# Performance work log

Hardware: AMD Instinct MI355X
Metric: run time of the kernel (lower is better)

## Reference

```python
import jax, jax.numpy as jnp
import numpy as np

EPS_CR = 0.5      # eps in coding rate
ETA = 0.5
LAMBDA_LAP = 0.3
LN_EPS = 1e-5


def setup_inputs() -> dict:
    key = jax.random.key(0)
    ks = jax.random.split(key, 8)
    n, in_dim, out_dim, d_sub, K1 = 8192, 256, 128, 64, 3
    H = jax.random.normal(ks[0], (n, in_dim), jnp.float32)
    hop_feats = jax.random.normal(ks[1], (K1, n, in_dim), jnp.float32)
    L = jax.random.normal(ks[2], (n, n), jnp.float32) * 0.01
    W_stack = jax.random.normal(ks[3], (K1, d_sub, in_dim), jnp.float32) * 0.05
    W_out = jax.random.normal(ks[4], (out_dim, in_dim), jnp.float32) * 0.05
    threshold = jnp.full((out_dim,), 0.05, jnp.float32)
    ln_gamma = jnp.ones((out_dim,), jnp.float32)
    ln_beta = jnp.zeros((out_dim,), jnp.float32)
    tau = jnp.asarray(1.0, jnp.float32)
    return {"H": H, "hop_feats": hop_feats, "L": L, "W_stack": W_stack,
            "W_out": W_out, "threshold": threshold, "ln_gamma": ln_gamma,
            "ln_beta": ln_beta, "tau": tau}


def reference(H, hop_feats, L, W_stack, W_out, threshold, ln_gamma, ln_beta, tau):
    n = H.shape[0]
    d = W_stack.shape[1]
    coeff = d / (n * EPS_CR * EPS_CR)
    # per-hop subspace projections: Z [K+1, n, d]
    Z = jnp.einsum('knf,kdf->knd', hop_feats, W_stack)
    # shared Gram M = I + coeff * Z^T Z  [K+1, d, d]
    G = jnp.einsum('knd,kne->kde', Z, Z)
    M = jnp.eye(d, dtype=Z.dtype)[None] + coeff * G
    # coding rates via batched slogdet
    _, logdet = jnp.linalg.slogdet(M)
    R = 0.5 * logdet                                    # [K+1]
    # delta_R: first entry is R[0], rest are successive diffs
    delta_R = R - jnp.concatenate([jnp.zeros((1,), R.dtype), R[:-1]])
    dR_norm = (delta_R - delta_R.mean()) / (jnp.std(delta_R, ddof=1) + 1e-6)
    w = jax.nn.softmax(dR_norm / tau)                   # [K+1]
    # coding-rate gradients: g_Z = coeff * Z @ M^{-1} via batched solve
    g_Z = coeff * jnp.linalg.solve(M, jnp.swapaxes(Z, 1, 2))  # [K+1, d, n]
    # g_H[k] = g_Z[k]^T @ W[k]; weighted sum over hops -> [n, in_dim]
    grad_contrib = jnp.einsum('k,kdn,kdf->nf', w, g_Z, W_stack)
    H_half = H + ETA * grad_contrib - ETA * LAMBDA_LAP * (L @ H)
    # in_dim != out_dim -> project
    H_pre = H_half @ W_out.T                            # [n, out_dim]
    thr = jnp.abs(threshold)[None, :]
    H_soft = jnp.sign(H_pre) * jnp.maximum(jnp.abs(H_pre) - thr, 0.0)
    # LayerNorm over last dim
    mu = H_soft.mean(-1, keepdims=True)
    var = jnp.mean((H_soft - mu) ** 2, -1, keepdims=True)
    H_out = (H_soft - mu) * jax.lax.rsqrt(var + LN_EPS) * ln_gamma + ln_beta
    return (H_out, w, jax.lax.stop_gradient(dR_norm), jax.lax.stop_gradient(delta_R))
```

## Files before the change

kernel.cpp:

```cpp
#include <hip/hip_runtime.h>
#include <hip/hip_bf16.h>
#include <math.h>


#define COEFF 0.03125f
#define SCL_LAP (-0.15f)

typedef __attribute__((ext_vector_type(8))) short short8;
typedef __attribute__((ext_vector_type(4))) float f32x4;

__device__ __forceinline__ unsigned short f2bf_bits(float f) {
  unsigned int u = __float_as_uint(f);
  unsigned int r = (u + 0x7fffu + ((u >> 16) & 1u)) >> 16;
  return (unsigned short)r;
}

__device__ __forceinline__ void gemm_body(
    const float* __restrict__ A, const float* __restrict__ B,
    int K, int lda, int ldb, int m0, int n0,
    float* As, float* Bs, float cc[4][4]) {
  const int tid = threadIdx.x;
  const int tx = tid & 15, ty = tid >> 4;
#pragma unroll
  for (int i = 0; i < 4; ++i)
#pragma unroll
    for (int j = 0; j < 4; ++j) cc[i][j] = 0.f;
  const int lr = tid >> 2, lc = (tid & 3) << 2;
  for (int k0 = 0; k0 < K; k0 += 16) {
    float4 av = *(const float4*)(A + (size_t)(m0 + lr) * lda + k0 + lc);
    As[(lc) * 68 + lr] = av.x; As[(lc + 1) * 68 + lr] = av.y;
    As[(lc + 2) * 68 + lr] = av.z; As[(lc + 3) * 68 + lr] = av.w;
    float4 bv = *(const float4*)(B + (size_t)(n0 + lr) * ldb + k0 + lc);
    Bs[(lc) * 68 + lr] = bv.x; Bs[(lc + 1) * 68 + lr] = bv.y;
    Bs[(lc + 2) * 68 + lr] = bv.z; Bs[(lc + 3) * 68 + lr] = bv.w;
    __syncthreads();
#pragma unroll
    for (int kk = 0; kk < 16; ++kk) {
      float4 a4 = *(const float4*)&As[kk * 68 + ty * 4];
      float4 b4 = *(const float4*)&Bs[kk * 68 + tx * 4];
      float a[4] = {a4.x, a4.y, a4.z, a4.w};
      float bb[4] = {b4.x, b4.y, b4.z, b4.w};
#pragma unroll
      for (int i = 0; i < 4; ++i)
#pragma unroll
        for (int j = 0; j < 4; ++j) cc[i][j] = fmaf(a[i], bb[j], cc[i][j]);
    }
    __syncthreads();
  }
}

__global__ __launch_bounds__(256) void front_kernel(
    const float* __restrict__ H, const float* __restrict__ hop,
    const float* __restrict__ Wst, const float* __restrict__ Wout,
    float* __restrict__ Hp, unsigned short* __restrict__ HpT,
    float* __restrict__ Zbuf, float* __restrict__ Gpart,
    float* __restrict__ Pb) {
  __shared__ __align__(16) float smem[4420];
  float* As = smem;
  float* Bs = smem + 1088;
  const int tid = threadIdx.x;
  const int tx = tid & 15, ty = tid >> 4;
  float cc[4][4];
  const int b = blockIdx.x;

  if (b < 256) {
    const int m0 = (b >> 1) * 64, n0 = (b & 1) * 64;
    gemm_body(H, Wout, 256, 256, 256, m0, n0, As, Bs, cc);
#pragma unroll
    for (int i = 0; i < 4; ++i) {
      float4 v = {cc[i][0], cc[i][1], cc[i][2], cc[i][3]};
      *(float4*)(Hp + (size_t)(m0 + ty * 4 + i) * 128 + n0 + tx * 4) = v;
    }
#pragma unroll
    for (int i = 0; i < 4; ++i)
#pragma unroll
      for (int j = 0; j < 4; ++j)
        smem[(ty * 4 + i) * 65 + tx * 4 + j] = cc[i][j];
    __syncthreads();
    const int c = tid >> 2, mb = (tid & 3) << 4;
    __attribute__((aligned(16))) unsigned short tmp[16];
#pragma unroll
    for (int t = 0; t < 16; ++t) tmp[t] = f2bf_bits(smem[(mb + t) * 65 + c]);
    unsigned short* dst = HpT + (size_t)(n0 + c) * 8192 + m0 + mb;
    *(uint4*)dst = *(const uint4*)&tmp[0];
    *(uint4*)(dst + 8) = *(const uint4*)&tmp[8];
  } else if (b < 640) {
    const int i2 = b - 256;
    const int k = i2 >> 7, mblk = i2 & 127;
    const int m0 = mblk * 64;
    gemm_body(hop + (size_t)k * 2097152, Wst + (size_t)k * 16384,
              256, 256, 256, m0, 0, As, Bs, cc);
#pragma unroll
    for (int i = 0; i < 4; ++i) {
      float4 v = {cc[i][0], cc[i][1], cc[i][2], cc[i][3]};
      *(float4*)(Zbuf + (size_t)(m0 + ty * 4 + i) * 192 + k * 64 + tx * 4) = v;
    }
#pragma unroll
    for (int i = 0; i < 4; ++i)
#pragma unroll
      for (int j = 0; j < 4; ++j)
        smem[(ty * 4 + i) * 68 + tx * 4 + j] = cc[i][j];
    __syncthreads();
    float g[4][4];
#pragma unroll
    for (int i = 0; i < 4; ++i)
#pragma unroll
      for (int j = 0; j < 4; ++j) g[i][j] = 0.f;
    const int d0 = tx * 4, e0 = ty * 4;
    for (int r = 0; r < 64; ++r) {
      float4 zd4 = *(const float4*)&smem[r * 68 + d0];
      float4 ze4 = *(const float4*)&smem[r * 68 + e0];
      float zd[4] = {zd4.x, zd4.y, zd4.z, zd4.w};
      float ze[4] = {ze4.x, ze4.y, ze4.z, ze4.w};
#pragma unroll
      for (int i = 0; i < 4; ++i)
#pragma unroll
        for (int j = 0; j < 4; ++j) g[i][j] = fmaf(zd[i], ze[j], g[i][j]);
    }
    float* gp = Gpart + ((size_t)k * 128 + mblk) * 4096;
#pragma unroll
    for (int i = 0; i < 4; ++i) {
      float4 v = {g[i][0], g[i][1], g[i][2], g[i][3]};
      *(float4*)(gp + (d0 + i) * 64 + e0) = v;
    }
  } else {
    const int i2 = b - 640;
    const int k = i2 >> 1;
    const int m0 = (i2 & 1) * 64;
    gemm_body(Wout, Wst + (size_t)k * 16384, 256, 256, 256, m0, 0, As, Bs, cc);
    float* P = Pb + (size_t)k * 8192;
#pragma unroll
    for (int i = 0; i < 4; ++i) {
      float4 v = {cc[i][0], cc[i][1], cc[i][2], cc[i][3]};
      *(float4*)(P + (size_t)(m0 + ty * 4 + i) * 64 + tx * 4) = v;
    }
  }
}

__global__ __launch_bounds__(256) void gsum_kernel(
    const float* __restrict__ Gpart, float* __restrict__ Gsum) {
  const int k = blockIdx.x >> 4;
  const int i = ((blockIdx.x & 15) << 8) + threadIdx.x;
  const float* gp = Gpart + (size_t)k * 128 * 4096 + i;
  float s0 = 0.f, s1 = 0.f, s2 = 0.f, s3 = 0.f;
  for (int bb = 0; bb < 128; bb += 4) {
    s0 += gp[(size_t)bb * 4096];
    s1 += gp[(size_t)(bb + 1) * 4096];
    s2 += gp[(size_t)(bb + 2) * 4096];
    s3 += gp[(size_t)(bb + 3) * 4096];
  }
  Gsum[(size_t)k * 4096 + i] = (s0 + s1) + (s2 + s3);
}

__device__ __forceinline__ float blocksum256(float v, volatile float* scr) {
#pragma unroll
  for (int o = 32; o; o >>= 1) v += __shfl_xor(v, o);
  __syncthreads();
  if ((threadIdx.x & 63) == 0) scr[threadIdx.x >> 6] = v;
  __syncthreads();
  return scr[0] + scr[1] + scr[2] + scr[3];
}

__device__ __forceinline__ void gemm64s(const float* X, const float* Y,
                                        float acc[4][4]) {
  const int tx = threadIdx.x & 15, ty = threadIdx.x >> 4;
#pragma unroll
  for (int i = 0; i < 4; ++i)
#pragma unroll
    for (int j = 0; j < 4; ++j) acc[i][j] = 0.f;
  for (int kk = 0; kk < 64; ++kk) {
    float4 a4 = *(const float4*)&X[kk * 64 + ty * 4];
    float4 b4 = *(const float4*)&Y[kk * 64 + tx * 4];
    float a[4] = {a4.x, a4.y, a4.z, a4.w};
    float bb[4] = {b4.x, b4.y, b4.z, b4.w};
#pragma unroll
    for (int i = 0; i < 4; ++i)
#pragma unroll
      for (int j = 0; j < 4; ++j) acc[i][j] = fmaf(a[i], bb[j], acc[i][j]);
  }
}

__device__ __forceinline__ void wb64(float* D, const float acc[4][4]) {
  const int tx = threadIdx.x & 15, ty = threadIdx.x >> 4;
#pragma unroll
  for (int i = 0; i < 4; ++i)
#pragma unroll
    for (int j = 0; j < 4; ++j) D[(ty * 4 + i) * 64 + tx * 4 + j] = acc[i][j];
}

__device__ __forceinline__ float dot64(const float* X, const float* Y, float* scr) {
  const int tx = threadIdx.x & 15, ty = threadIdx.x >> 4;
  float v = 0.f;
#pragma unroll
  for (int i = 0; i < 4; ++i)
#pragma unroll
    for (int j = 0; j < 4; ++j) {
      int idx = (ty * 4 + i) * 64 + tx * 4 + j;
      v += X[idx] * Y[idx];
    }
  return blocksum256(v, scr);
}

__global__ __launch_bounds__(256) void fused_big(
    const float* __restrict__ Lp, const unsigned short* __restrict__ HpT,
    float* __restrict__ Pbuf, const float* __restrict__ Gsum,
    float* __restrict__ Minv, float* __restrict__ Rout) {
  __shared__ __align__(16) float smem[12304];
  const int tid = threadIdx.x;

  if (blockIdx.x >= 3) {
    unsigned short (*As)[40] = (unsigned short(*)[40])smem;
    unsigned short (*Bs)[40] = (unsigned short(*)[40])(smem + 2560);
    const int g = blockIdx.x - 3;
    const int m0 = (g & 63) * 128;
    const int split = g >> 6;
    const int kbase = split * 1024;
    const int wave = tid >> 6, lane = tid & 63;
    const int ar = tid >> 1, ah = (tid & 1) * 16;
    const size_t lrow = (size_t)(m0 + ar) * 8192;
    const size_t brow = (size_t)ar * 8192;
    f32x4 acc[2][8];
#pragma unroll
    for (int i = 0; i < 2; ++i)
#pragma unroll
      for (int j = 0; j < 8; ++j) acc[i][j] = (f32x4){0.f, 0.f, 0.f, 0.f};
    float4 apf[4];
    uint4 bpf[2];
    {
      const float* ap = Lp + lrow + kbase + ah;
      apf[0] = *(const float4*)(ap); apf[1] = *(const float4*)(ap + 4);
      apf[2] = *(const float4*)(ap + 8); apf[3] = *(const float4*)(ap + 12);
      const unsigned short* bp = HpT + brow + kbase + ah;
      bpf[0] = *(const uint4*)(bp); bpf[1] = *(const uint4*)(bp + 8);
    }
    const int quad = lane >> 4, mcol = lane & 15;
    for (int step = 0; step < 32; ++step) {
      __syncthreads();
      {
        __attribute__((aligned(16))) unsigned short tmp[16];
        const float* f = (const float*)apf;
#pragma unroll
        for (int i = 0; i < 16; ++i) tmp[i] = f2bf_bits(f[i]);
        *(uint4*)&As[ar][ah] = *(const uint4*)&tmp[0];
        *(uint4*)&As[ar][ah + 8] = *(const uint4*)&tmp[8];
        *(uint4*)&Bs[ar][ah] = bpf[0];
        *(uint4*)&Bs[ar][ah + 8] = bpf[1];
      }
      __syncthreads();
      if (step < 31) {
        int kc = kbase + (step + 1) * 32;
        const float* ap = Lp + lrow + kc + ah;
        apf[0] = *(const float4*)(ap); apf[1] = *(const float4*)(ap + 4);
        apf[2] = *(const float4*)(ap + 8); apf[3] = *(const float4*)(ap + 12);
        const unsigned short* bp = HpT + brow + kc + ah;
        bpf[0] = *(const uint4*)(bp); bpf[1] = *(const uint4*)(bp + 8);
      }
      short8 af0 = *(const short8*)&As[wave * 32 + mcol][quad * 8];
      short8 af1 = *(const short8*)&As[wave * 32 + 16 + mcol][quad * 8];
#pragma unroll
      for (int nt = 0; nt < 8; ++nt) {
        short8 bf = *(const short8*)&Bs[nt * 16 + mcol][quad * 8];
        acc[0][nt] = __builtin_amdgcn_mfma_f32_16x16x32_bf16(af0, bf, acc[0][nt], 0, 0, 0);
        acc[1][nt] = __builtin_amdgcn_mfma_f32_16x16x32_bf16(af1, bf, acc[1][nt], 0, 0, 0);
      }
    }
    float* P = Pbuf + (size_t)split * 1048576;
#pragma unroll
    for (int mt = 0; mt < 2; ++mt)
#pragma unroll
      for (int nt = 0; nt < 8; ++nt)
#pragma unroll
        for (int r = 0; r < 4; ++r) {
          int grow = m0 + wave * 32 + mt * 16 + quad * 4 + r;
          int gcol = nt * 16 + mcol;
          P[(size_t)grow * 128 + gcol] = acc[mt][nt][r];
        }
    return;
  }

  const int k = blockIdx.x;
  float* B0 = smem;
  float* B1 = smem + 4096;
  float* B2 = smem + 8192;
  float* scr = smem + 12288;
  for (int i = tid; i < 4096; i += 256) {
    B0[i] = COEFF * Gsum[(size_t)k * 4096 + i] + ((i >> 6) == (i & 63) ? 1.f : 0.f);
  }
  __syncthreads();
  if (tid < 64) {
    float rs = 0.f, dg = B0[tid * 65];
    for (int j = 0; j < 64; ++j) rs += fabsf(B0[j * 64 + tid]);
    float lo = 2.f * dg - rs, hi = rs;
#pragma unroll
    for (int o = 32; o; o >>= 1) {
      lo = fminf(lo, __shfl_xor(lo, o));
      hi = fmaxf(hi, __shfl_xor(hi, o));
    }
    if (tid == 0) scr[4] = 0.5f * (fmaxf(lo, 1.f) + hi);
  }
  __syncthreads();
  const float alpha = scr[4], inva = 1.f / alpha;
  for (int i = tid; i < 4096; i += 256) {
    int r = i >> 6, c = i & 63;
    B0[i] = B0[i] * inva - (r == c ? 1.f : 0.f);
  }
  __syncthreads();
  const int tx = tid & 15, ty = tid >> 4;
  float v1 = 0.f, v2 = 0.f;
#pragma unroll
  for (int i = 0; i < 4; ++i)
#pragma unroll
    for (int j = 0; j < 4; ++j) {
      int r = ty * 4 + i, c = tx * 4 + j;
      float e = B0[r * 64 + c];
      if (r == c) v1 += e;
      v2 += e * e;
    }
  float t1 = blocksum256(v1, scr);
  float t2 = blocksum256(v2, scr);
  float acc[4][4];
  gemm64s(B0, B0, acc); __syncthreads(); wb64(B1, acc); __syncthreads();
  float t3 = dot64(B1, B0, scr);
  float t4 = dot64(B1, B1, scr);
  gemm64s(B1, B0, acc); __syncthreads(); wb64(B2, acc); __syncthreads();
  float t5 = dot64(B2, B1, scr);
  float t6 = dot64(B2, B2, scr);
  gemm64s(B1, B1, acc);
  {
    float v7 = 0.f, v8 = 0.f;
#pragma unroll
    for (int i = 0; i < 4; ++i)
#pragma unroll
      for (int j = 0; j < 4; ++j) {
        int idx = (ty * 4 + i) * 64 + tx * 4 + j;
        v7 += acc[i][j] * B2[idx];
        v8 += acc[i][j] * acc[i][j];
      }
    float t7 = blocksum256(v7, scr);
    float t8 = blocksum256(v8, scr);
    if (tid == 0) {
      float ld = 64.f * logf(alpha) + t1 - t2 * 0.5f + t3 / 3.f - t4 * 0.25f
                 + t5 * 0.2f - t6 / 6.f + t7 / 7.f - t8 * 0.125f;
      Rout[k] = 0.5f * ld;
    }
  }
  for (int i = tid; i < 4096; i += 256) {
    int r = i >> 6, c = i & 63;
    B1[i] = (r == c ? 1.f : 0.f) - B0[i];
  }
  __syncthreads();
  for (int it = 0; it < 2; ++it) {
    gemm64s(B0, B1, acc);
    __syncthreads();
    {
#pragma unroll
      for (int i = 0; i < 4; ++i)
#pragma unroll
        for (int j = 0; j < 4; ++j) {
          int idx = (ty * 4 + i) * 64 + tx * 4 + j;
          B2[idx] = acc[i][j] + B1[idx];
        }
    }
    __syncthreads();
    gemm64s(B1, B2, acc);
    __syncthreads();
    {
#pragma unroll
      for (int i = 0; i < 4; ++i)
#pragma unroll
        for (int j = 0; j < 4; ++j) {
          int idx = (ty * 4 + i) * 64 + tx * 4 + j;
          B1[idx] = 2.f * B1[idx] - acc[i][j];
        }
    }
    __syncthreads();
  }
  for (int i = tid; i < 4096; i += 256) Minv[k * 4096 + i] = B1[i] * inva;
}

__global__ __launch_bounds__(256) void qtw_kernel(
    const float* __restrict__ Pb, const float* __restrict__ Minv,
    const float* __restrict__ R, const float* __restrict__ tauP,
    float* __restrict__ QT, float* __restrict__ tail) {
  __shared__ __align__(16) float XT[4096];
  __shared__ __align__(16) float Y[4096];
  __shared__ float wsh;
  const int tid = threadIdx.x;
  const int k = blockIdx.x >> 1;
  const int m0 = (blockIdx.x & 1) * 64;
  if (tid == 0) {
    float R0 = R[0], R1 = R[1], R2 = R[2];
    float d0 = R0, d1 = R1 - R0, d2 = R2 - R1;
    float mean = (d0 + d1 + d2) * (1.f / 3.f);
    float e0 = d0 - mean, e1 = d1 - mean, e2 = d2 - mean;
    float sd = sqrtf((e0 * e0 + e1 * e1 + e2 * e2) * 0.5f) + 1e-6f;
    float n0 = e0 / sd, n1 = e1 / sd, n2 = e2 / sd;
    float tau = tauP[0];
    float x0 = n0 / tau, x1 = n1 / tau, x2 = n2 / tau;
    float mx = fmaxf(x0, fmaxf(x1, x2));
    float w0 = expf(x0 - mx), w1 = expf(x1 - mx), w2 = expf(x2 - mx);
    float s = w0 + w1 + w2;
    w0 /= s; w1 /= s; w2 /= s;
    wsh = 0.015625f * (k == 0 ? w0 : (k == 1 ? w1 : w2));
    if (blockIdx.x == 0) {
      tail[0] = w0; tail[1] = w1; tail[2] = w2;
      tail[3] = n0; tail[4] = n1; tail[5] = n2;
      tail[6] = d0; tail[7] = d1; tail[8] = d2;
    }
  }
  {
    const int m = tid >> 2, c4 = (tid & 3) << 4;
    const float* src = Pb + (size_t)k * 8192 + (size_t)(m0 + m) * 64 + c4;
#pragma unroll
    for (int t = 0; t < 16; t += 4) {
      float4 v = *(const float4*)(src + t);
      XT[(c4 + t) * 64 + m] = v.x;
      XT[(c4 + t + 1) * 64 + m] = v.y;
      XT[(c4 + t + 2) * 64 + m] = v.z;
      XT[(c4 + t + 3) * 64 + m] = v.w;
    }
    for (int t = tid * 4; t < 4096; t += 1024)
      *(float4*)&Y[t] = *(const float4*)(Minv + (size_t)k * 4096 + t);
  }
  __syncthreads();
  float acc[4][4];
  gemm64s(XT, Y, acc);
  const float s = wsh;
  const int tx = tid & 15, ty = tid >> 4;
#pragma unroll
  for (int i = 0; i < 4; ++i) {
    float4 v = {s * acc[i][0], s * acc[i][1], s * acc[i][2], s * acc[i][3]};
    *(float4*)(QT + (size_t)(m0 + ty * 4 + i) * 192 + k * 64 + tx * 4) = v;
  }
}

__global__ __launch_bounds__(256) void back_kernel(
    const float* __restrict__ Zbuf, const float* __restrict__ QT,
    const float* __restrict__ Hp, const float* __restrict__ Pbuf,
    const float* __restrict__ thr, const float* __restrict__ gamma,
    const float* __restrict__ beta, float* __restrict__ out) {
  __shared__ __align__(16) float As[16][36];
  __shared__ __align__(16) float Bs[16][132];
  const int tid = threadIdx.x;
  const int tx = tid & 15, ty = tid >> 4;
  const int m0 = blockIdx.x * 32;
  float cc[2][8];
#pragma unroll
  for (int i = 0; i < 2; ++i)
#pragma unroll
    for (int j = 0; j < 8; ++j) cc[i][j] = 0.f;
  const int lr = tid >> 2, lc = (tid & 3) << 2;
  const int jr = tid >> 1, jc = (tid & 1) << 3;
  for (int k0 = 0; k0 < 192; k0 += 16) {
    if (tid < 128) {
      float4 av = *(const float4*)(Zbuf + (size_t)(m0 + lr) * 192 + k0 + lc);
      As[lc][lr] = av.x; As[lc + 1][lr] = av.y;
      As[lc + 2][lr] = av.z; As[lc + 3][lr] = av.w;
    }
    {
      const float* q = QT + (size_t)jr * 192 + k0 + jc;
      float4 b0 = *(const float4*)(q);
      float4 b1 = *(const float4*)(q + 4);
      Bs[jc][jr] = b0.x; Bs[jc + 1][jr] = b0.y;
      Bs[jc + 2][jr] = b0.z; Bs[jc + 3][jr] = b0.w;
      Bs[jc + 4][jr] = b1.x; Bs[jc + 5][jr] = b1.y;
      Bs[jc + 6][jr] = b1.z; Bs[jc + 7][jr] = b1.w;
    }
    __syncthreads();
#pragma unroll
    for (int kk = 0; kk < 16; ++kk) {
      float2 a2 = *(const float2*)&As[kk][ty * 2];
      float4 b4a = *(const float4*)&Bs[kk][tx * 8];
      float4 b4b = *(const float4*)&Bs[kk][tx * 8 + 4];
      float bb[8] = {b4a.x, b4a.y, b4a.z, b4a.w, b4b.x, b4b.y, b4b.z, b4b.w};
#pragma unroll
      for (int j = 0; j < 8; ++j) {
        cc[0][j] = fmaf(a2.x, bb[j], cc[0][j]);
        cc[1][j] = fmaf(a2.y, bb[j], cc[1][j]);
      }
    }
    __syncthreads();
  }
  const float4 tA = *(const float4*)(thr + tx * 8);
  const float4 tB = *(const float4*)(thr + tx * 8 + 4);
  const float tv[8] = {fabsf(tA.x), fabsf(tA.y), fabsf(tA.z), fabsf(tA.w),
                       fabsf(tB.x), fabsf(tB.y), fabsf(tB.z), fabsf(tB.w)};
  const float4 gA = *(const float4*)(gamma + tx * 8);
  const float4 gB = *(const float4*)(gamma + tx * 8 + 4);
  const float gv[8] = {gA.x, gA.y, gA.z, gA.w, gB.x, gB.y, gB.z, gB.w};
  const float4 bA = *(const float4*)(beta + tx * 8);
  const float4 bB = *(const float4*)(beta + tx * 8 + 4);
  const float bv[8] = {bA.x, bA.y, bA.z, bA.w, bB.x, bB.y, bB.z, bB.w};
  float sres[2][8], mean[2], inv[2];
#pragma unroll
  for (int i = 0; i < 2; ++i) {
    const size_t off = (size_t)(m0 + ty * 2 + i) * 128 + tx * 8;
    float4 h0 = *(const float4*)(Hp + off);
    float4 h1 = *(const float4*)(Hp + off + 4);
    float p[8] = {0.f, 0.f, 0.f, 0.f, 0.f, 0.f, 0.f, 0.f};
#pragma unroll
    for (int sp = 0; sp < 8; ++sp) {
      const float* pb = Pbuf + (size_t)sp * 1048576 + off;
      float4 q0 = *(const float4*)(pb);
      float4 q1 = *(const float4*)(pb + 4);
      p[0] += q0.x; p[1] += q0.y; p[2] += q0.z; p[3] += q0.w;
      p[4] += q1.x; p[5] += q1.y; p[6] += q1.z; p[7] += q1.w;
    }
    const float hv[8] = {h0.x, h0.y, h0.z, h0.w, h1.x, h1.y, h1.z, h1.w};
    float sum = 0.f;
#pragma unroll
    for (int j = 0; j < 8; ++j) {
      float x = cc[i][j] + hv[j] + SCL_LAP * p[j];
      float a = fmaxf(fabsf(x) - tv[j], 0.f);
      float sx = (x >= 0.f) ? a : -a;
      sres[i][j] = sx;
      sum += sx;
    }
#pragma unroll
    for (int o = 1; o < 16; o <<= 1) sum += __shfl_xor(sum, o);
    mean[i] = sum * (1.f / 128.f);
    float ss = 0.f;
#pragma unroll
    for (int j = 0; j < 8; ++j) {
      float dd = sres[i][j] - mean[i];
      ss += dd * dd;
    }
#pragma unroll
    for (int o = 1; o < 16; o <<= 1) ss += __shfl_xor(ss, o);
    inv[i] = rsqrtf(ss * (1.f / 128.f) + 1e-5f);
  }
#pragma unroll
  for (int i = 0; i < 2; ++i) {
    const size_t off = (size_t)(m0 + ty * 2 + i) * 128 + tx * 8;
    float o8[8];
#pragma unroll
    for (int j = 0; j < 8; ++j)
      o8[j] = (sres[i][j] - mean[i]) * inv[i] * gv[j] + bv[j];
    float4 v0 = {o8[0], o8[1], o8[2], o8[3]};
    float4 v1 = {o8[4], o8[5], o8[6], o8[7]};
    *(float4*)(out + off) = v0;
    *(float4*)(out + off + 4) = v1;
  }
}

extern "C" void kernel_launch(void* const* d_in, const int* in_sizes, int n_in,
                              void* d_out, int out_size, void* d_ws, size_t ws_size,
                              hipStream_t stream) {
  const float* H = (const float*)d_in[0];
  const float* hop = (const float*)d_in[1];
  const float* L = (const float*)d_in[2];
  const float* Wst = (const float*)d_in[3];
  const float* Wout = (const float*)d_in[4];
  const float* thr = (const float*)d_in[5];
  const float* gamma = (const float*)d_in[6];
  const float* beta = (const float*)d_in[7];
  const float* tau = (const float*)d_in[8];
  float* out = (float*)d_out;

  float* ws = (float*)d_ws;
  float* Zbuf = ws;
  float* Hp = Zbuf + 1572864;
  float* Gpart = Hp + 1048576;
  float* Gsum = Gpart + 1572864;
  float* Minv = Gsum + 12288;
  float* Rb = Minv + 12288;
  float* Pb = Rb + 16;
  float* QT = Pb + 24576;
  float* Pbuf = QT + 24576;
  unsigned short* HpT = (unsigned short*)(Pbuf + 8388608);

  front_kernel<<<dim3(646), 256, 0, stream>>>(H, hop, Wst, Wout,
                                              Hp, HpT, Zbuf, Gpart, Pb);
  gsum_kernel<<<dim3(48), 256, 0, stream>>>(Gpart, Gsum);
  fused_big<<<dim3(515), 256, 0, stream>>>(L, HpT, Pbuf, Gsum, Minv, Rb);
  qtw_kernel<<<dim3(6), 256, 0, stream>>>(Pb, Minv, Rb, tau, QT, out + 1048576);
  back_kernel<<<dim3(256), 256, 0, stream>>>(Zbuf, QT, Hp, Pbuf,
                                             thr, gamma, beta, out);

  (void)in_sizes; (void)n_in; (void)out_size; (void)ws_size;
}
```

Baseline: 493.1 us.

## Enlarge front GEMM tiles, fold Gram partial sum into solver, reorder split-K mapping

```diff
diff --git a/kernel.cpp b/kernel.cpp
--- a/kernel.cpp
+++ b/kernel.cpp
@@ -13,40 +13,6 @@
   unsigned int u = __float_as_uint(f);
   unsigned int r = (u + 0x7fffu + ((u >> 16) & 1u)) >> 16;
   return (unsigned short)r;
-}
-
-__device__ __forceinline__ void gemm_body(
-    const float* __restrict__ A, const float* __restrict__ B,
-    int K, int lda, int ldb, int m0, int n0,
-    float* As, float* Bs, float cc[4][4]) {
-  const int tid = threadIdx.x;
-  const int tx = tid & 15, ty = tid >> 4;
-#pragma unroll
-  for (int i = 0; i < 4; ++i)
-#pragma unroll
-    for (int j = 0; j < 4; ++j) cc[i][j] = 0.f;
-  const int lr = tid >> 2, lc = (tid & 3) << 2;
-  for (int k0 = 0; k0 < K; k0 += 16) {
-    float4 av = *(const float4*)(A + (size_t)(m0 + lr) * lda + k0 + lc);
-    As[(lc) * 68 + lr] = av.x; As[(lc + 1) * 68 + lr] = av.y;
-    As[(lc + 2) * 68 + lr] = av.z; As[(lc + 3) * 68 + lr] = av.w;
-    float4 bv = *(const float4*)(B + (size_t)(n0 + lr) * ldb + k0 + lc);
-    Bs[(lc) * 68 + lr] = bv.x; Bs[(lc + 1) * 68 + lr] = bv.y;
-    Bs[(lc + 2) * 68 + lr] = bv.z; Bs[(lc + 3) * 68 + lr] = bv.w;
-    __syncthreads();
-#pragma unroll
-    for (int kk = 0; kk < 16; ++kk) {
-      float4 a4 = *(const float4*)&As[kk * 68 + ty * 4];
-      float4 b4 = *(const float4*)&Bs[kk * 68 + tx * 4];
-      float a[4] = {a4.x, a4.y, a4.z, a4.w};
-      float bb[4] = {b4.x, b4.y, b4.z, b4.w};
-#pragma unroll
-      for (int i = 0; i < 4; ++i)
-#pragma unroll
-        for (int j = 0; j < 4; ++j) cc[i][j] = fmaf(a[i], bb[j], cc[i][j]);
-    }
-    __syncthreads();
-  }
 }
 
 __global__ __launch_bounds__(256) void front_kernel(
@@ -55,61 +21,80 @@
     float* __restrict__ Hp, unsigned short* __restrict__ HpT,
     float* __restrict__ Zbuf, float* __restrict__ Gpart,
     float* __restrict__ Pb) {
-  __shared__ __align__(16) float smem[4420];
+  __shared__ __align__(16) float smem[8704];
   float* As = smem;
-  float* Bs = smem + 1088;
+  float* Bs = smem + 2112;
   const int tid = threadIdx.x;
   const int tx = tid & 15, ty = tid >> 4;
-  float cc[4][4];
   const int b = blockIdx.x;
 
-  if (b < 256) {
-    const int m0 = (b >> 1) * 64, n0 = (b & 1) * 64;
-    gemm_body(H, Wout, 256, 256, 256, m0, n0, As, Bs, cc);
-#pragma unroll
-    for (int i = 0; i < 4; ++i) {
-      float4 v = {cc[i][0], cc[i][1], cc[i][2], cc[i][3]};
-      *(float4*)(Hp + (size_t)(m0 + ty * 4 + i) * 128 + n0 + tx * 4) = v;
-    }
+  const float* A;
+  const float* B;
+  int m0 = 0, k_id = 0, n_off = 0, mode;
+  if (b < 192) {
+    mode = 0; k_id = b >> 6; m0 = (b & 63) * 128;
+    A = hop + (size_t)k_id * 2097152;
+    B = Wst + (size_t)k_id * 16384;
+  } else if (b < 320) {
+    mode = 1; int i2 = b - 192;
+    m0 = (i2 >> 1) * 128; n_off = (i2 & 1) * 64;
+    A = H; B = Wout + (size_t)n_off * 256;
+  } else {
+    mode = 2; k_id = b - 320; m0 = 0;
+    A = Wout; B = Wst + (size_t)k_id * 16384;
+  }
+
+  float acc[8][4];
+#pragma unroll
+  for (int i = 0; i < 8; ++i)
+#pragma unroll
+    for (int j = 0; j < 4; ++j) acc[i][j] = 0.f;
+
+  const int arow = tid >> 1, ak = (tid & 1) * 8;
+  const int brow = tid >> 2, bk = (tid & 3) * 4;
+  for (int k0 = 0; k0 < 256; k0 += 16) {
+    float4 a0 = *(const float4*)(A + (size_t)(m0 + arow) * 256 + k0 + ak);
+    float4 a1 = *(const float4*)(A + (size_t)(m0 + arow) * 256 + k0 + ak + 4);
+    float4 bv = *(const float4*)(B + (size_t)brow * 256 + k0 + bk);
+    __syncthreads();
+    As[(ak + 0) * 132 + arow] = a0.x; As[(ak + 1) * 132 + arow] = a0.y;
+    As[(ak + 2) * 132 + arow] = a0.z; As[(ak + 3) * 132 + arow] = a0.w;
+    As[(ak + 4) * 132 + arow] = a1.x; As[(ak + 5) * 132 + arow] = a1.y;
+    As[(ak + 6) * 132 + arow] = a1.z; As[(ak + 7) * 132 + arow] = a1.w;
+    Bs[(bk + 0) * 68 + brow] = bv.x; Bs[(bk + 1) * 68 + brow] = bv.y;
+    Bs[(bk + 2) * 68 + brow] = bv.z; Bs[(bk + 3) * 68 + brow] = bv.w;
+    __syncthreads();
+#pragma unroll
+    for (int kk = 0; kk < 16; ++kk) {
+      float4 x0 = *(const float4*)&As[kk * 132 + ty * 8];
+      float4 x1 = *(const float4*)&As[kk * 132 + ty * 8 + 4];
+      float4 y4 = *(const float4*)&Bs[kk * 68 + tx * 4];
+      float a8[8] = {x0.x, x0.y, x0.z, x0.w, x1.x, x1.y, x1.z, x1.w};
+      float b4[4] = {y4.x, y4.y, y4.z, y4.w};
+#pragma unroll
+      for (int i = 0; i < 8; ++i)
+#pragma unroll
+        for (int j = 0; j < 4; ++j) acc[i][j] = fmaf(a8[i], b4[j], acc[i][j]);
+    }
+  }
+  __syncthreads();
+
+  if (mode == 0) {
+#pragma unroll
+    for (int i = 0; i < 8; ++i) {
+      float4 v = {acc[i][0], acc[i][1], acc[i][2], acc[i][3]};
+      *(float4*)(Zbuf + (size_t)(m0 + ty * 8 + i) * 192 + k_id * 64 + tx * 4) = v;
+      *(float4*)&smem[(ty * 8 + i) * 68 + tx * 4] = v;
+    }
+    __syncthreads();
+    float g[4][4];
 #pragma unroll
     for (int i = 0; i < 4; ++i)
 #pragma unroll
-      for (int j = 0; j < 4; ++j)
-        smem[(ty * 4 + i) * 65 + tx * 4 + j] = cc[i][j];
-    __syncthreads();
-    const int c = tid >> 2, mb = (tid & 3) << 4;
-    __attribute__((aligned(16))) unsigned short tmp[16];
-#pragma unroll
-    for (int t = 0; t < 16; ++t) tmp[t] = f2bf_bits(smem[(mb + t) * 65 + c]);
-    unsigned short* dst = HpT + (size_t)(n0 + c) * 8192 + m0 + mb;
-    *(uint4*)dst = *(const uint4*)&tmp[0];
-    *(uint4*)(dst + 8) = *(const uint4*)&tmp[8];
-  } else if (b < 640) {
-    const int i2 = b - 256;
-    const int k = i2 >> 7, mblk = i2 & 127;
-    const int m0 = mblk * 64;
-    gemm_body(hop + (size_t)k * 2097152, Wst + (size_t)k * 16384,
-              256, 256, 256, m0, 0, As, Bs, cc);
-#pragma unroll
-    for (int i = 0; i < 4; ++i) {
-      float4 v = {cc[i][0], cc[i][1], cc[i][2], cc[i][3]};
-      *(float4*)(Zbuf + (size_t)(m0 + ty * 4 + i) * 192 + k * 64 + tx * 4) = v;
-    }
-#pragma unroll
-    for (int i = 0; i < 4; ++i)
-#pragma unroll
-      for (int j = 0; j < 4; ++j)
-        smem[(ty * 4 + i) * 68 + tx * 4 + j] = cc[i][j];
-    __syncthreads();
-    float g[4][4];
-#pragma unroll
-    for (int i = 0; i < 4; ++i)
-#pragma unroll
       for (int j = 0; j < 4; ++j) g[i][j] = 0.f;
-    const int d0 = tx * 4, e0 = ty * 4;
-    for (int r = 0; r < 64; ++r) {
-      float4 zd4 = *(const float4*)&smem[r * 68 + d0];
-      float4 ze4 = *(const float4*)&smem[r * 68 + e0];
+    for (int r = 0; r < 128; ++r) {
+      float4 zd4 = *(const float4*)&smem[r * 68 + ty * 4];
+      float4 ze4 = *(const float4*)&smem[r * 68 + tx * 4];
       float zd[4] = {zd4.x, zd4.y, zd4.z, zd4.w};
       float ze[4] = {ze4.x, ze4.y, ze4.z, ze4.w};
 #pragma unroll
@@ -117,39 +102,37 @@
 #pragma unroll
         for (int j = 0; j < 4; ++j) g[i][j] = fmaf(zd[i], ze[j], g[i][j]);
     }
-    float* gp = Gpart + ((size_t)k * 128 + mblk) * 4096;
+    float* gp = Gpart + (size_t)(k_id * 64 + (b & 63)) * 4096;
 #pragma unroll
     for (int i = 0; i < 4; ++i) {
       float4 v = {g[i][0], g[i][1], g[i][2], g[i][3]};
-      *(float4*)(gp + (d0 + i) * 64 + e0) = v;
-    }
+      *(float4*)(gp + (ty * 4 + i) * 64 + tx * 4) = v;
+    }
+  } else if (mode == 1) {
+#pragma unroll
+    for (int i = 0; i < 8; ++i) {
+      float4 v = {acc[i][0], acc[i][1], acc[i][2], acc[i][3]};
+      *(float4*)(Hp + (size_t)(m0 + ty * 8 + i) * 128 + n_off + tx * 4) = v;
+      *(float4*)&smem[(ty * 8 + i) * 68 + tx * 4] = v;
+    }
+    __syncthreads();
+    const int nn = tid >> 2, mc = (tid & 3) * 32;
+    __attribute__((aligned(16))) unsigned short tmp[32];
+#pragma unroll
+    for (int mm = 0; mm < 32; ++mm) tmp[mm] = f2bf_bits(smem[(mc + mm) * 68 + nn]);
+    unsigned short* dst = HpT + (size_t)(n_off + nn) * 8192 + m0 + mc;
+    *(uint4*)(dst) = *(const uint4*)&tmp[0];
+    *(uint4*)(dst + 8) = *(const uint4*)&tmp[8];
+    *(uint4*)(dst + 16) = *(const uint4*)&tmp[16];
+    *(uint4*)(dst + 24) = *(const uint4*)&tmp[24];
   } else {
-    const int i2 = b - 640;
-    const int k = i2 >> 1;
-    const int m0 = (i2 & 1) * 64;
-    gemm_body(Wout, Wst + (size_t)k * 16384, 256, 256, 256, m0, 0, As, Bs, cc);
-    float* P = Pb + (size_t)k * 8192;
-#pragma unroll
-    for (int i = 0; i < 4; ++i) {
-      float4 v = {cc[i][0], cc[i][1], cc[i][2], cc[i][3]};
-      *(float4*)(P + (size_t)(m0 + ty * 4 + i) * 64 + tx * 4) = v;
-    }
-  }
-}
-
-__global__ __launch_bounds__(256) void gsum_kernel(
-    const float* __restrict__ Gpart, float* __restrict__ Gsum) {
-  const int k = blockIdx.x >> 4;
-  const int i = ((blockIdx.x & 15) << 8) + threadIdx.x;
-  const float* gp = Gpart + (size_t)k * 128 * 4096 + i;
-  float s0 = 0.f, s1 = 0.f, s2 = 0.f, s3 = 0.f;
-  for (int bb = 0; bb < 128; bb += 4) {
-    s0 += gp[(size_t)bb * 4096];
-    s1 += gp[(size_t)(bb + 1) * 4096];
-    s2 += gp[(size_t)(bb + 2) * 4096];
-    s3 += gp[(size_t)(bb + 3) * 4096];
-  }
-  Gsum[(size_t)k * 4096 + i] = (s0 + s1) + (s2 + s3);
+    float* P = Pb + (size_t)k_id * 8192;
+#pragma unroll
+    for (int i = 0; i < 8; ++i) {
+      float4 v = {acc[i][0], acc[i][1], acc[i][2], acc[i][3]};
+      *(float4*)(P + (size_t)(ty * 8 + i) * 64 + tx * 4) = v;
+    }
+  }
 }
 
 __device__ __forceinline__ float blocksum256(float v, volatile float* scr) {
@@ -203,7 +186,7 @@
 
 __global__ __launch_bounds__(256) void fused_big(
     const float* __restrict__ Lp, const unsigned short* __restrict__ HpT,
-    float* __restrict__ Pbuf, const float* __restrict__ Gsum,
+    float* __restrict__ Pbuf, const float* __restrict__ Gpart,
     float* __restrict__ Minv, float* __restrict__ Rout) {
   __shared__ __align__(16) float smem[12304];
   const int tid = threadIdx.x;
@@ -212,8 +195,8 @@
     unsigned short (*As)[40] = (unsigned short(*)[40])smem;
     unsigned short (*Bs)[40] = (unsigned short(*)[40])(smem + 2560);
     const int g = blockIdx.x - 3;
-    const int m0 = (g & 63) * 128;
-    const int split = g >> 6;
+    const int split = g & 7;
+    const int m0 = (g >> 3) * 128;
     const int kbase = split * 1024;
     const int wave = tid >> 6, lane = tid & 63;
     const int ar = tid >> 1, ah = (tid & 1) * 16;
@@ -283,8 +266,19 @@
   float* B1 = smem + 4096;
   float* B2 = smem + 8192;
   float* scr = smem + 12288;
-  for (int i = tid; i < 4096; i += 256) {
-    B0[i] = COEFF * Gsum[(size_t)k * 4096 + i] + ((i >> 6) == (i & 63) ? 1.f : 0.f);
+  for (int i4 = tid * 4; i4 < 4096; i4 += 1024) {
+    const float* gp = Gpart + (size_t)k * 64 * 4096 + i4;
+    float s0 = 0.f, s1 = 0.f, s2 = 0.f, s3 = 0.f;
+    for (int bb2 = 0; bb2 < 64; ++bb2) {
+      float4 v = *(const float4*)(gp + (size_t)bb2 * 4096);
+      s0 += v.x; s1 += v.y; s2 += v.z; s3 += v.w;
+    }
+    float sv[4] = {s0, s1, s2, s3};
+#pragma unroll
+    for (int e = 0; e < 4; ++e) {
+      int i = i4 + e;
+      B0[i] = COEFF * sv[e] + ((i >> 6) == (i & 63) ? 1.f : 0.f);
+    }
   }
   __syncthreads();
   if (tid < 64) {
@@ -561,18 +555,16 @@
   float* Zbuf = ws;
   float* Hp = Zbuf + 1572864;
   float* Gpart = Hp + 1048576;
-  float* Gsum = Gpart + 1572864;
-  float* Minv = Gsum + 12288;
+  float* Minv = Gpart + 786432;
   float* Rb = Minv + 12288;
   float* Pb = Rb + 16;
   float* QT = Pb + 24576;
   float* Pbuf = QT + 24576;
   unsigned short* HpT = (unsigned short*)(Pbuf + 8388608);
 
-  front_kernel<<<dim3(646), 256, 0, stream>>>(H, hop, Wst, Wout,
+  front_kernel<<<dim3(323), 256, 0, stream>>>(H, hop, Wst, Wout,
                                               Hp, HpT, Zbuf, Gpart, Pb);
-  gsum_kernel<<<dim3(48), 256, 0, stream>>>(Gpart, Gsum);
-  fused_big<<<dim3(515), 256, 0, stream>>>(L, HpT, Pbuf, Gsum, Minv, Rb);
+  fused_big<<<dim3(515), 256, 0, stream>>>(L, HpT, Pbuf, Gpart, Minv, Rb);
   qtw_kernel<<<dim3(6), 256, 0, stream>>>(Pb, Minv, Rb, tau, QT, out + 1048576);
   back_kernel<<<dim3(256), 256, 0, stream>>>(Zbuf, QT, Hp, Pbuf,
                                              thr, gamma, beta, out);
```

New measurement: 513.3 us. 4.1% more time.
